# Kernel optimization log

Measured on AMD Instinct MI355X. Metric: run time of the kernel, lower is better.

## Reference

```python
import jax, jax.numpy as jnp
import numpy as np

HEAD = 8

def _mvn(x, eps=1e-5):
    # per-(batch,channel) mean/std over spatial dims; torch .var default is unbiased (ddof=1)
    mean = jnp.mean(x, axis=(2, 3), keepdims=True)
    var = jnp.var(x, axis=(2, 3), ddof=1, keepdims=True) + eps
    return (x - mean) / jnp.sqrt(var)

def _conv1x1(x, w, b):
    return jnp.einsum('bchw,oc->bohw', x, w) + b[None, :, None, None]

def _block_heads(x, p):
    # non-overlapping unfold (kernel==stride==p): pure reshape; matches torch unfold ordering
    b, c, h, w = x.shape
    y = x.reshape(b, c, h // p, p, w // p, p).transpose(0, 1, 2, 4, 3, 5)
    n, r = (h // p) * (w // p), p * p
    return y.reshape(b, HEAD, c // HEAD, n, r)

def _unblock(x, p, h, w):
    # inverse of non-overlapping unfold (fold with kernel==stride)
    b, c, n, r = x.shape
    y = x.reshape(b, c, h // p, w // p, p, p).transpose(0, 1, 2, 4, 3, 5)
    return y.reshape(b, c, h, w)

def setup_inputs() -> dict:
    key = jax.random.key(0)
    ks = jax.random.split(key, 12)
    B, C, H, W = 4, 512, 64, 64
    wmat = lambda k: jax.random.normal(k, (C, C), jnp.float32) * 0.05
    zb = jnp.zeros((C,), jnp.float32)
    return {
        'content': jax.random.normal(ks[0], (B, C, H, W), jnp.float32),
        'style': jax.random.normal(ks[1], (B, C, H, W), jnp.float32),
        'q_w': wmat(ks[2]), 'q_b': zb,
        'k_w': wmat(ks[3]), 'k_b': zb,
        'v_w': wmat(ks[4]), 'v_b': zb,
        'q2_w': wmat(ks[5]), 'q2_b': zb,
        'k2_w': wmat(ks[6]), 'k2_b': zb,
        'v2_w': wmat(ks[7]), 'v2_b': zb,
        'f1_w': wmat(ks[8]), 'f1_b': zb,
        'f2_w': wmat(ks[9]), 'f2_b': zb,
        'sim_alpha': jnp.ones((1,), jnp.float32),
        'sim_beta': jnp.zeros((1,), jnp.float32),
        'layer': 3,
    }

def reference(content, style, q_w, q_b, k_w, k_b, v_w, v_b, q2_w, q2_b, k2_w, k2_b,
              v2_w, v2_b, f1_w, f1_b, f2_w, f2_b, sim_alpha, sim_beta, layer):
    region = 8 if int(layer) in (3, 4) else 4
    b, c, h, w = content.shape
    nc = _mvn(content)
    ns = _mvn(style)
    DA_q = _block_heads(_conv1x1(nc, q_w, q_b), region)      # [b,H,ch,n,r]
    DA_k = _block_heads(_conv1x1(ns, k_w, k_b), region)
    DA_v = _block_heads(_conv1x1(style, v_w, v_b), region)
    PA_q = _block_heads(_conv1x1(nc, q2_w, q2_b), region)
    PA_k = _block_heads(_conv1x1(ns, k2_w, k2_b), region)
    PA_v = _block_heads(_conv1x1(style, v2_w, v2_b), region)
    r = region * region
    n = DA_q.shape[3]
    # --- distinctiveness attention: mean-center clustering + sigmoid-weighted aggregation ---
    DA_k_c = jnp.mean(DA_k, axis=-1)                          # [b,H,ch,n]
    DA_v_c = jnp.mean(DA_v, axis=-1)
    dis = jnp.einsum('bhcx,bhcxy->bhxy', DA_k_c, DA_k)
    sim = jax.nn.sigmoid(sim_beta + sim_alpha * dis)          # [b,H,n,r]
    DA_k_agg = (jnp.einsum('bhxy,bhcxy->bhcx', sim, DA_k) + DA_k_c) / (r + 1)
    DA_v_agg = (jnp.einsum('bhxy,bhcxy->bhcx', sim, DA_v) + DA_v_c) / (r + 1)
    logits = jnp.einsum('bhcxy,bhcz->bhyxz', DA_q, DA_k_agg)  # [b,H,r,n,n]
    scores = jax.nn.softmax(logits, axis=-1)
    DA = jnp.einsum('bhyxz,bhcz->bhcxy', scores, DA_v_agg)    # [b,H,ch,n,r]
    DA_ub = _unblock(DA.reshape(b, c, n, r), region, h, w)
    # --- point attention: argmax NN block matching, then intra-block attention ---
    PA1 = jnp.einsum('bhcxy,bhczy->bhxz', PA_q, PA_k)         # [b,H,n,n]
    idx = jnp.argmax(PA1, axis=-1)                            # [b,H,n]
    idx_b = jnp.broadcast_to(idx[:, :, None, :, None], PA_k.shape)
    PA_k_rs = jnp.take_along_axis(PA_k, idx_b, axis=3)
    PA_v_rs = jnp.take_along_axis(PA_v, idx_b, axis=3)
    logits2 = jnp.einsum('bhcxy,bhcxz->bhxyz', PA_q, PA_k_rs) # [b,H,n,r,r]
    scores2 = jax.nn.softmax(logits2, axis=-1)
    PA = jnp.einsum('bhxyz,bhcxz->bhcxy', scores2, PA_v_rs)
    PA_ub = _unblock(PA.reshape(b, c, n, r), region, h, w)
    O = _conv1x1(DA_ub, f1_w, f1_b) + _conv1x1(PA_ub, f2_w, f2_b)
    return O + content
```

## Files before the change

### kernel.cpp

```cpp
#include <hip/hip_runtime.h>

typedef unsigned short u16;
typedef unsigned int   u32;
typedef _Float16       f16;

typedef f16   f16x8 __attribute__((ext_vector_type(8)));
typedef f16   f16x4 __attribute__((ext_vector_type(4)));
typedef float f32x4 __attribute__((ext_vector_type(4)));

__device__ __forceinline__ f32x4 mfma16(f16x8 a, f16x8 b, f32x4 c){
  return __builtin_amdgcn_mfma_f32_16x16x32_f16(a, b, c, 0, 0, 0);
}

__device__ __forceinline__ void glds16(const f16* g, f16* l){
  __builtin_amdgcn_global_load_lds(
      (const __attribute__((address_space(1))) void*)g,
      (__attribute__((address_space(3))) void*)l, 16, 0, 0);
}

__global__ __launch_bounds__(256) void k_mvn_stats(
    const float* __restrict__ content, const float* __restrict__ style,
    float* __restrict__ stats)
{
  const int src = blockIdx.x >> 11;
  const int row = blockIdx.x & 2047;
  const float* xp = (src ? style : content) + (size_t)row * 4096;
  const int t = threadIdx.x;
  double s = 0.0, ss = 0.0;
  for(int i = t * 4; i < 4096; i += 1024){
    float4 v = *(const float4*)(xp + i);
    s  += (double)v.x + (double)v.y + (double)v.z + (double)v.w;
    ss += (double)v.x * v.x + (double)v.y * v.y + (double)v.z * v.z + (double)v.w * v.w;
  }
  #pragma unroll
  for(int off = 32; off > 0; off >>= 1){
    s  += __shfl_xor(s, off);
    ss += __shfl_xor(ss, off);
  }
  __shared__ double sh[8];
  const int wid = t >> 6;
  if((t & 63) == 0){ sh[wid] = s; sh[4 + wid] = ss; }
  __syncthreads();
  if(t == 0){
    double S  = sh[0] + sh[1] + sh[2] + sh[3];
    double SS = sh[4] + sh[5] + sh[6] + sh[7];
    float mean = (float)(S * (1.0 / 4096.0));
    float var  = (float)((SS - S * S * (1.0 / 4096.0)) * (1.0 / 4095.0));
    stats[src * 4096 + row] = mean;
    stats[src * 4096 + 2048 + row] = rsqrtf(var + 1e-5f);
  }
}

__global__ __launch_bounds__(256) void k_prep_w_all(
    const float* __restrict__ qW,  const float* __restrict__ qB,
    const float* __restrict__ kW,  const float* __restrict__ kB,
    const float* __restrict__ q2W, const float* __restrict__ q2B,
    const float* __restrict__ k2W, const float* __restrict__ k2B,
    const float* __restrict__ vW,  const float* __restrict__ vB,
    const float* __restrict__ v2W, const float* __restrict__ v2B,
    const float* __restrict__ f1W, const float* __restrict__ f2W,
    const float* __restrict__ stats,
    f16* __restrict__ qw, f16* __restrict__ kw,
    f16* __restrict__ q2wh, f16* __restrict__ q2wl,
    f16* __restrict__ k2wh, f16* __restrict__ k2wl,
    f16* __restrict__ vw, f16* __restrict__ v2w,
    f16* __restrict__ f1w, f16* __restrict__ f2w,
    float* __restrict__ biasp)
{
  const int t = threadIdx.x;
  int rid = blockIdx.x * 32 + (t >> 3);
  const float *W; const float *B = nullptr;
  int side = -1, b = 0, o;
  f16 *oh; f16 *ol = nullptr; float* bs = nullptr;
  if(rid < 2048){
    b = rid >> 9; o = rid & 511;
    W = qW; B = qB; side = 0;
    oh = qw + (size_t)(b * 512 + o) * 512;
    bs = biasp + 0 * 2048 + b * 512 + o;
  } else if(rid < 4096){
    rid -= 2048; b = rid >> 9; o = rid & 511;
    W = kW; B = kB; side = 1;
    oh = kw + (size_t)(b * 512 + o) * 512;
    bs = biasp + 1 * 2048 + b * 512 + o;
  } else if(rid < 6144){
    rid -= 4096; b = rid >> 9; o = rid & 511;
    W = q2W; B = q2B; side = 0;
    oh = q2wh + (size_t)(b * 512 + o) * 512;
    ol = q2wl + (size_t)(b * 512 + o) * 512;
    bs = biasp + 4 * 2048 + b * 512 + o;
  } else if(rid < 8192){
    rid -= 6144; b = rid >> 9; o = rid & 511;
    W = k2W; B = k2B; side = 1;
    oh = k2wh + (size_t)(b * 512 + o) * 512;
    ol = k2wl + (size_t)(b * 512 + o) * 512;
    bs = biasp + 5 * 2048 + b * 512 + o;
  } else if(rid < 8704){
    o = rid - 8192; W = vW; B = vB;
    oh = vw + (size_t)o * 512;
    bs = biasp + 2 * 2048 + o;
  } else if(rid < 9216){
    o = rid - 8704; W = v2W; B = v2B;
    oh = v2w + (size_t)o * 512;
    bs = biasp + 3 * 2048 + o;
  } else if(rid < 9728){
    o = rid - 9216; W = f1W;
    oh = f1w + (size_t)o * 512;
  } else {
    o = rid - 9728; W = f2W;
    oh = f2w + (size_t)o * 512;
  }
  const float* mp = (side >= 0) ? stats + side * 4096 + b * 512 : nullptr;
  const float* rp = (side >= 0) ? mp + 2048 : nullptr;
  const int c0 = (t & 7) * 64;
  float dot = 0.f;
  #pragma unroll
  for(int i = 0; i < 64; i += 8){
    int c = c0 + i;
    float w[8];
    *(float4*)(w)     = *(const float4*)(W + (size_t)o * 512 + c);
    *(float4*)(w + 4) = *(const float4*)(W + (size_t)o * 512 + c + 4);
    f16x8 h8, l8;
    #pragma unroll
    for(int j = 0; j < 8; j++){
      float wp = w[j];
      if(side >= 0){
        float r = rp[c + j];
        dot += wp * mp[c + j] * r;
        wp *= r;
      }
      f16 h = (f16)wp;
      h8[j] = h; l8[j] = (f16)(wp - (float)h);
    }
    *(f16x8*)(oh + c) = h8;
    if(ol) *(f16x8*)(ol + c) = l8;
  }
  if(bs){
    dot += __shfl_xor(dot, 1); dot += __shfl_xor(dot, 2); dot += __shfl_xor(dot, 4);
    if((t & 7) == 0) *bs = B[o] - dot;
  }
}

__global__ __launch_bounds__(256) void k_prep_x(
    const float* __restrict__ content, const float* __restrict__ style,
    f16* __restrict__ cth, f16* __restrict__ ctl,
    f16* __restrict__ sth, f16* __restrict__ stl)
{
  const int side = blockIdx.z;
  const int b = blockIdx.y;
  const int s0 = blockIdx.x * 128;
  const float* Xb = (side ? style : content) + (size_t)b * 512 * 4096;
  f16* Oh = (side ? sth : cth) + (size_t)b * 4096 * 512;
  f16* Ol = (side ? stl : ctl) + (size_t)b * 4096 * 512;
  __shared__ float Xs[32][132];
  const int t = threadIdx.x;
  const int s = t >> 1, half = t & 1;
  for(int cc = 0; cc < 512; cc += 32){
    __syncthreads();
    #pragma unroll
    for(int u = 0; u < 4; u++){
      int q = t + u * 256;
      int row = q >> 5, f4 = q & 31;
      float4 v = *(const float4*)(Xb + (size_t)(cc + row) * 4096 + s0 + f4 * 4);
      *(float4*)(&Xs[row][f4 * 4]) = v;
    }
    __syncthreads();
    f16x8 h0, h1, l0, l1;
    #pragma unroll
    for(int i = 0; i < 8; i++){
      float x = Xs[half * 16 + i][s];
      f16 h = (f16)x; h0[i] = h; l0[i] = (f16)(x - (float)h);
    }
    #pragma unroll
    for(int i = 0; i < 8; i++){
      float x = Xs[half * 16 + 8 + i][s];
      f16 h = (f16)x; h1[i] = h; l1[i] = (f16)(x - (float)h);
    }
    size_t o = (size_t)(s0 + s) * 512 + cc + half * 16;
    *(f16x8*)(Oh + o) = h0; *(f16x8*)(Oh + o + 8) = h1;
    *(f16x8*)(Ol + o) = l0; *(f16x8*)(Ol + o + 8) = l1;
  }
}

__global__ __launch_bounds__(256) void k_convT(
    const f16* __restrict__ Xt, const f16* __restrict__ Wp,
    const float* __restrict__ bias, int bw, f16* __restrict__ Out)
{
  const int b = blockIdx.z;
  const int o0 = blockIdx.y * 128;
  const int s0 = blockIdx.x * 128;
  const f16* Xb = Xt + (size_t)b * 4096 * 512;
  const f16* Wb = Wp + (bw ? (size_t)b * 262144 : 0);
  const float* bp = bias + (bw ? b * 512 : 0);
  f16* Ob = Out + (size_t)b * 512 * 4096;
  __shared__ f16 As[4096];
  __shared__ f16 Bs[4096];
  const int t = threadIdx.x;
  const int lane = t & 63, wid = t >> 6;
  const int wm = (wid >> 1) * 64, wn = (wid & 1) * 64;
  const int lr = lane & 15, lg = lane >> 4;
  const int sr = lane >> 2, sc = lane & 3;
  f32x4 acc[4][4] = {};
  for(int kk = 0; kk < 512; kk += 32){
    __syncthreads();
    #pragma unroll
    for(int i = 0; i < 2; i++){
      int r0 = wid * 32 + i * 16;
      int r = r0 + sr;
      int cs = (sc ^ ((r >> 1) & 3)) << 3;
      glds16(Wb + (size_t)(o0 + r) * 512 + kk + cs, As + r0 * 32);
      glds16(Xb + (size_t)(s0 + r) * 512 + kk + cs, Bs + r0 * 32);
    }
    __syncthreads();
    f16x8 av[4], bv[4];
    #pragma unroll
    for(int mi = 0; mi < 4; mi++){
      int row = wm + mi * 16 + lr;
      av[mi] = *(const f16x8*)(As + row * 32 + ((lg ^ ((row >> 1) & 3)) << 3));
    }
    #pragma unroll
    for(int ni = 0; ni < 4; ni++){
      int row = wn + ni * 16 + lr;
      bv[ni] = *(const f16x8*)(Bs + row * 32 + ((lg ^ ((row >> 1) & 3)) << 3));
    }
    #pragma unroll
    for(int mi = 0; mi < 4; mi++){
      #pragma unroll
      for(int ni = 0; ni < 4; ni++)
        acc[mi][ni] = mfma16(av[mi], bv[ni], acc[mi][ni]);
    }
  }
  #pragma unroll
  for(int mi = 0; mi < 4; mi++){
    #pragma unroll
    for(int ni = 0; ni < 4; ni++){
      #pragma unroll
      for(int j = 0; j < 4; j++){
        int o = o0 + wm + mi * 16 + lg * 4 + j;
        int s = s0 + wn + ni * 16 + lr;
        Ob[(size_t)o * 4096 + s] = (f16)(acc[mi][ni][j] + bp[o]);
      }
    }
  }
}

__global__ __launch_bounds__(256) void k_conv3out(
    const f16* __restrict__ Xt,
    const f16* __restrict__ Wk, const f16* __restrict__ Wv, const f16* __restrict__ Wv2,
    const float* __restrict__ biasp,
    f16* __restrict__ Ok, f16* __restrict__ Ov, f16* __restrict__ Ov2)
{
  const int b = blockIdx.z;
  const int seg = blockIdx.y >> 2;
  const int o0 = (blockIdx.y & 3) * 128;
  const int s0 = blockIdx.x * 128;
  const f16* Xb = Xt + (size_t)b * 4096 * 512;
  const f16* Wb = seg == 0 ? Wk + (size_t)b * 262144 : (seg == 1 ? Wv : Wv2);
  const float* bp = biasp + (seg == 0 ? 1 * 2048 + b * 512 : (seg == 1 ? 2 * 2048 : 3 * 2048));
  f16* Ob = (seg == 0 ? Ok : (seg == 1 ? Ov : Ov2)) + (size_t)b * 512 * 4096;
  __shared__ f16 As[4096];
  __shared__ f16 Bs[4096];
  const int t = threadIdx.x;
  const int lane = t & 63, wid = t >> 6;
  const int wm = (wid >> 1) * 64, wn = (wid & 1) * 64;
  const int lr = lane & 15, lg = lane >> 4;
  const int sr = lane >> 2, sc = lane & 3;
  f32x4 acc[4][4] = {};
  for(int kk = 0; kk < 512; kk += 32){
    __syncthreads();
    #pragma unroll
    for(int i = 0; i < 2; i++){
      int r0 = wid * 32 + i * 16;
      int r = r0 + sr;
      int cs = (sc ^ ((r >> 1) & 3)) << 3;
      glds16(Wb + (size_t)(o0 + r) * 512 + kk + cs, As + r0 * 32);
      glds16(Xb + (size_t)(s0 + r) * 512 + kk + cs, Bs + r0 * 32);
    }
    __syncthreads();
    f16x8 av[4], bv[4];
    #pragma unroll
    for(int mi = 0; mi < 4; mi++){
      int row = wm + mi * 16 + lr;
      av[mi] = *(const f16x8*)(As + row * 32 + ((lg ^ ((row >> 1) & 3)) << 3));
    }
    #pragma unroll
    for(int ni = 0; ni < 4; ni++){
      int row = wn + ni * 16 + lr;
      bv[ni] = *(const f16x8*)(Bs + row * 32 + ((lg ^ ((row >> 1) & 3)) << 3));
    }
    #pragma unroll
    for(int mi = 0; mi < 4; mi++){
      #pragma unroll
      for(int ni = 0; ni < 4; ni++)
        acc[mi][ni] = mfma16(av[mi], bv[ni], acc[mi][ni]);
    }
  }
  #pragma unroll
  for(int mi = 0; mi < 4; mi++){
    #pragma unroll
    for(int ni = 0; ni < 4; ni++){
      #pragma unroll
      for(int j = 0; j < 4; j++){
        int o = o0 + wm + mi * 16 + lg * 4 + j;
        int s = s0 + wn + ni * 16 + lr;
        Ob[(size_t)o * 4096 + s] = (f16)(acc[mi][ni][j] + bp[o]);
      }
    }
  }
}

__global__ __launch_bounds__(256) void k_convT3(
    const f16* __restrict__ Xh, const f16* __restrict__ Xl,
    const f16* __restrict__ Wh, const f16* __restrict__ Wl,
    const float* __restrict__ bias, f16* __restrict__ Oh, f16* __restrict__ Ol)
{
  const int b = blockIdx.z;
  const int o0 = blockIdx.y * 128;
  const int s0 = blockIdx.x * 128;
  const f16* Xhb = Xh + (size_t)b * 4096 * 512;
  const f16* Xlb = Xl + (size_t)b * 4096 * 512;
  const f16* Whb = Wh + (size_t)b * 262144;
  const f16* Wlb = Wl + (size_t)b * 262144;
  const float* bp = bias + b * 512;
  f16* Ohb = Oh + (size_t)b * 512 * 4096;
  f16* Olb = Ol + (size_t)b * 512 * 4096;
  __shared__ f16 Ah[4096], Al[4096], Bh[4096], Bl[4096];
  const int t = threadIdx.x;
  const int lane = t & 63, wid = t >> 6;
  const int wm = (wid >> 1) * 64, wn = (wid & 1) * 64;
  const int lr = lane & 15, lg = lane >> 4;
  const int sr = lane >> 2, sc = lane & 3;
  f32x4 acc[4][4] = {};
  for(int kk = 0; kk < 512; kk += 32){
    __syncthreads();
    #pragma unroll
    for(int i = 0; i < 2; i++){
      int r0 = wid * 32 + i * 16;
      int r = r0 + sr;
      int cs = (sc ^ ((r >> 1) & 3)) << 3;
      size_t wsrc = (size_t)(o0 + r) * 512 + kk + cs;
      size_t xsrc = (size_t)(s0 + r) * 512 + kk + cs;
      glds16(Whb + wsrc, Ah + r0 * 32);
      glds16(Wlb + wsrc, Al + r0 * 32);
      glds16(Xhb + xsrc, Bh + r0 * 32);
      glds16(Xlb + xsrc, Bl + r0 * 32);
    }
    __syncthreads();
    f16x8 ah[4], alo[4], bh[4], blo[4];
    #pragma unroll
    for(int mi = 0; mi < 4; mi++){
      int row = wm + mi * 16 + lr;
      int off = row * 32 + ((lg ^ ((row >> 1) & 3)) << 3);
      ah[mi]  = *(const f16x8*)(Ah + off);
      alo[mi] = *(const f16x8*)(Al + off);
    }
    #pragma unroll
    for(int ni = 0; ni < 4; ni++){
      int row = wn + ni * 16 + lr;
      int off = row * 32 + ((lg ^ ((row >> 1) & 3)) << 3);
      bh[ni]  = *(const f16x8*)(Bh + off);
      blo[ni] = *(const f16x8*)(Bl + off);
    }
    #pragma unroll
    for(int mi = 0; mi < 4; mi++){
      #pragma unroll
      for(int ni = 0; ni < 4; ni++){
        f32x4 a = acc[mi][ni];
        a = mfma16(ah[mi],  bh[ni],  a);
        a = mfma16(ah[mi],  blo[ni], a);
        a = mfma16(alo[mi], bh[ni],  a);
        acc[mi][ni] = a;
      }
    }
  }
  #pragma unroll
  for(int mi = 0; mi < 4; mi++){
    #pragma unroll
    for(int ni = 0; ni < 4; ni++){
      #pragma unroll
      for(int j = 0; j < 4; j++){
        int o = o0 + wm + mi * 16 + lg * 4 + j;
        int s = s0 + wn + ni * 16 + lr;
        float v = acc[mi][ni][j] + bp[o];
        f16 h = (f16)v;
        Ohb[(size_t)o * 4096 + s] = h;
        Olb[(size_t)o * 4096 + s] = (f16)(v - (float)h);
      }
    }
  }
}

__global__ __launch_bounds__(256) void k_da1(
    const f16* __restrict__ K, const f16* __restrict__ V,
    const float* __restrict__ alpha_p, const float* __restrict__ beta_p,
    float* __restrict__ kagg, float* __restrict__ vagg)
{
  const int hw = blockIdx.x;
  const int xcd = hw & 7, i = hw >> 3;
  const int g = xcd * 32 + (i >> 3);
  const int bh = g >> 3;
  const int x  = (g & 7) * 8 + (i & 7);
  const f16* Kb = K + (size_t)bh * 64 * 4096;
  const f16* Vb = V + (size_t)bh * 64 * 4096;
  __shared__ float kl[64][65];
  __shared__ float vl[64][65];
  __shared__ float kc[64], vc[64], simv[64];
  const int t = threadIdx.x;
  const int c = t >> 2, yp = t & 3;
  const int xb = (x >> 3) * 512 + (x & 7) * 8;
  #pragma unroll
  for(int u = 0; u < 2; u++){
    int yh = yp * 2 + u;
    f16x8 k8 = *(const f16x8*)(Kb + (size_t)c * 4096 + xb + yh * 64);
    f16x8 v8 = *(const f16x8*)(Vb + (size_t)c * 4096 + xb + yh * 64);
    #pragma unroll
    for(int j = 0; j < 8; j++){
      kl[c][yh * 8 + j] = (float)k8[j];
      vl[c][yh * 8 + j] = (float)v8[j];
    }
  }
  __syncthreads();
  float sk = 0.f, sv = 0.f;
  for(int yy = yp * 16; yy < yp * 16 + 16; yy++){ sk += kl[c][yy]; sv += vl[c][yy]; }
  sk += __shfl_xor(sk, 1); sk += __shfl_xor(sk, 2);
  sv += __shfl_xor(sv, 1); sv += __shfl_xor(sv, 2);
  if(yp == 0){ kc[c] = sk * (1.f / 64.f); vc[c] = sv * (1.f / 64.f); }
  __syncthreads();
  const int y = t >> 2, cp = t & 3;
  float d = 0.f;
  for(int cc = cp * 16; cc < cp * 16 + 16; cc++) d += kc[cc] * kl[cc][y];
  d += __shfl_xor(d, 1); d += __shfl_xor(d, 2);
  if(cp == 0) simv[y] = 1.f / (1.f + expf(-(beta_p[0] + alpha_p[0] * d)));
  __syncthreads();
  float ak = 0.f, av = 0.f;
  for(int yy = yp * 16; yy < yp * 16 + 16; yy++){
    float sm = simv[yy];
    ak += sm * kl[c][yy]; av += sm * vl[c][yy];
  }
  ak += __shfl_xor(ak, 1); ak += __shfl_xor(ak, 2);
  av += __shfl_xor(av, 1); av += __shfl_xor(av, 2);
  if(yp == 0){
    size_t o = ((size_t)bh * 64 + x) * 64 + c;
    kagg[o] = (ak + kc[c]) * (1.f / 65.f);
    vagg[o] = (av + vc[c]) * (1.f / 65.f);
  }
}

__global__ __launch_bounds__(256) void k_da2(
    const f16* __restrict__ Q, const float* __restrict__ kagg,
    const float* __restrict__ vagg, f16* __restrict__ OutT)
{
  const int bh = blockIdx.x >> 4;
  const int s0 = (blockIdx.x & 15) << 8;
  const int b_ = bh >> 3, hd = bh & 7;
  const f16* Qb = Q + (size_t)bh * 64 * 4096;
  f16* Ot = OutT + (size_t)b_ * 4096 * 512 + hd * 64;

  __shared__ __align__(16) f16 Qt[256][72];
  __shared__ __align__(16) f16 Kt[64][72];
  __shared__ __align__(16) f16 Vt[64][72];
  const int t = threadIdx.x;
  const int lane = t & 63, w = t >> 6;
  const int lr = lane & 15, lg = lane >> 4;

  {
    const int so = t & 31;
    #pragma unroll
    for(int pass = 0; pass < 8; pass++){
      int c = (t >> 5) + pass * 8;
      f16x8 q8 = *(const f16x8*)(Qb + (size_t)c * 4096 + s0 + so * 8);
      #pragma unroll
      for(int j = 0; j < 8; j++){
        int s = so * 8 + j;
        int col = (((c >> 3) ^ (s & 7)) << 3) | (c & 7);
        Qt[s][col] = q8[j];
      }
    }
  }
  {
    const int z = t >> 2, c0 = (t & 3) * 16;
    #pragma unroll
    for(int u = 0; u < 4; u++){
      float4 v = *(const float4*)(kagg + (size_t)bh * 4096 + z * 64 + c0 + u * 4);
      float vv[4] = {v.x, v.y, v.z, v.w};
      #pragma unroll
      for(int j = 0; j < 4; j++){
        int c = c0 + u * 4 + j;
        int col = (((c >> 3) ^ (z & 7)) << 3) | (c & 7);
        Kt[z][col] = (f16)vv[j];
      }
    }
    #pragma unroll
    for(int u = 0; u < 4; u++){
      float4 v = *(const float4*)(vagg + (size_t)bh * 4096 + z * 64 + c0 + u * 4);
      float vv[4] = {v.x, v.y, v.z, v.w};
      #pragma unroll
      for(int j = 0; j < 4; j++){
        int c = c0 + u * 4 + j;
        int col = (((z >> 3) ^ (c & 7)) << 3) | (z & 7);
        Vt[c][col] = (f16)vv[j];
      }
    }
  }
  __syncthreads();

  f32x4 acc[4][4] = {};
  #pragma unroll
  for(int kc = 0; kc < 2; kc++){
    f16x8 af[4], bf[4];
    #pragma unroll
    for(int mi = 0; mi < 4; mi++){
      int row = w * 64 + mi * 16 + lr;
      af[mi] = *(const f16x8*)(&Qt[row][(((kc * 4 + lg) ^ (row & 7)) << 3)]);
    }
    #pragma unroll
    for(int ni = 0; ni < 4; ni++){
      int row = ni * 16 + lr;
      bf[ni] = *(const f16x8*)(&Kt[row][(((kc * 4 + lg) ^ (row & 7)) << 3)]);
    }
    #pragma unroll
    for(int mi = 0; mi < 4; mi++){
      #pragma unroll
      for(int ni = 0; ni < 4; ni++)
        acc[mi][ni] = mfma16(af[mi], bf[ni], acc[mi][ni]);
    }
  }

  #pragma unroll
  for(int mi = 0; mi < 4; mi++){
    #pragma unroll
    for(int j = 0; j < 4; j++){
      float v0 = acc[mi][0][j], v1 = acc[mi][1][j], v2 = acc[mi][2][j], v3 = acc[mi][3][j];
      float m = fmaxf(fmaxf(v0, v1), fmaxf(v2, v3));
      m = fmaxf(m, __shfl_xor(m, 1)); m = fmaxf(m, __shfl_xor(m, 2));
      m = fmaxf(m, __shfl_xor(m, 4)); m = fmaxf(m, __shfl_xor(m, 8));
      float e0 = expf(v0 - m), e1 = expf(v1 - m), e2 = expf(v2 - m), e3 = expf(v3 - m);
      float sm = e0 + e1 + e2 + e3;
      sm += __shfl_xor(sm, 1); sm += __shfl_xor(sm, 2);
      sm += __shfl_xor(sm, 4); sm += __shfl_xor(sm, 8);
      float inv = 1.f / sm;
      float ev[4] = {e0, e1, e2, e3};
      int row = w * 64 + mi * 16 + lg * 4 + j;
      #pragma unroll
      for(int ni = 0; ni < 4; ni++){
        int z = lr + 16 * ni;
        int col = (((z >> 3) ^ (row & 7)) << 3) | (z & 7);
        Qt[row][col] = (f16)(ev[ni] * inv);
      }
    }
  }

  f32x4 acc2[4][4] = {};
  #pragma unroll
  for(int kc = 0; kc < 2; kc++){
    f16x8 af[4], bf[4];
    #pragma unroll
    for(int mi = 0; mi < 4; mi++){
      int row = w * 64 + mi * 16 + lr;
      af[mi] = *(const f16x8*)(&Qt[row][(((kc * 4 + lg) ^ (row & 7)) << 3)]);
    }
    #pragma unroll
    for(int ni = 0; ni < 4; ni++){
      int row = ni * 16 + lr;
      bf[ni] = *(const f16x8*)(&Vt[row][(((kc * 4 + lg) ^ (row & 7)) << 3)]);
    }
    #pragma unroll
    for(int mi = 0; mi < 4; mi++){
      #pragma unroll
      for(int ni = 0; ni < 4; ni++)
        acc2[mi][ni] = mfma16(af[mi], bf[ni], acc2[mi][ni]);
    }
  }

  #pragma unroll
  for(int mi = 0; mi < 4; mi++){
    #pragma unroll
    for(int j = 0; j < 4; j++){
      size_t srow = (size_t)(s0 + w * 64 + mi * 16 + lg * 4 + j) * 512;
      #pragma unroll
      for(int ni = 0; ni < 4; ni++)
        Ot[srow + ni * 16 + lr] = (f16)acc2[mi][ni][j];
    }
  }
}

__global__ __launch_bounds__(256) void k_pa1(
    const f16* __restrict__ Qh, const f16* __restrict__ Ql,
    const f16* __restrict__ Kh, const f16* __restrict__ Kl,
    float* __restrict__ pa1p)
{
  const int slice = blockIdx.x & 7;
  const int bh = blockIdx.x >> 3;
  const size_t base = (size_t)bh * 64 * 4096;
  __shared__ f16 Ah[2][64][72], Al[2][64][72], Bh[2][64][72], Bl[2][64][72];
  const int t = threadIdx.x;
  const int lane = t & 63, wid = t >> 6;
  const int wm = (wid >> 1) * 32, wn = (wid & 1) * 32;
  const int lr = lane & 15, lg = lane >> 4;
  f32x4 acc[2][2] = {};
  for(int chunk = 0; chunk < 4; chunk++){
    const int c0 = slice * 8 + chunk * 2;
    __syncthreads();
    #pragma unroll
    for(int cc = 0; cc < 2; cc++){
      size_t cbase = base + (size_t)(c0 + cc) * 4096;
      #pragma unroll
      for(int u = 0; u < 2; u++){
        int e = u * 256 + t;
        int x = e >> 3, yh = e & 7;
        size_t src = cbase + (size_t)((x >> 3) * 512 + (x & 7) * 8 + yh * 64);
        int dst = yh * 8;
        *(f16x8*)(&Ah[cc][x][dst]) = *(const f16x8*)(Qh + src);
        *(f16x8*)(&Al[cc][x][dst]) = *(const f16x8*)(Ql + src);
        *(f16x8*)(&Bh[cc][x][dst]) = *(const f16x8*)(Kh + src);
        *(f16x8*)(&Bl[cc][x][dst]) = *(const f16x8*)(Kl + src);
      }
    }
    __syncthreads();
    #pragma unroll
    for(int cc = 0; cc < 2; cc++){
      #pragma unroll
      for(int kc = 0; kc < 2; kc++){
        f16x8 ah[2], alo[2], bh[2], blo[2];
        #pragma unroll
        for(int mi = 0; mi < 2; mi++){
          ah[mi]  = *(const f16x8*)(&Ah[cc][wm + mi * 16 + lr][kc * 32 + lg * 8]);
          alo[mi] = *(const f16x8*)(&Al[cc][wm + mi * 16 + lr][kc * 32 + lg * 8]);
        }
        #pragma unroll
        for(int ni = 0; ni < 2; ni++){
          bh[ni]  = *(const f16x8*)(&Bh[cc][wn + ni * 16 + lr][kc * 32 + lg * 8]);
          blo[ni] = *(const f16x8*)(&Bl[cc][wn + ni * 16 + lr][kc * 32 + lg * 8]);
        }
        #pragma unroll
        for(int mi = 0; mi < 2; mi++){
          #pragma unroll
          for(int ni = 0; ni < 2; ni++){
            f32x4 a = acc[mi][ni];
            a = mfma16(ah[mi],  bh[ni],  a);
            a = mfma16(ah[mi],  blo[ni], a);
            a = mfma16(alo[mi], bh[ni],  a);
            acc[mi][ni] = a;
          }
        }
      }
    }
  }
  float* outp = pa1p + ((size_t)bh * 8 + slice) * 4096;
  #pragma unroll
  for(int mi = 0; mi < 2; mi++){
    #pragma unroll
    for(int ni = 0; ni < 2; ni++){
      #pragma unroll
      for(int j = 0; j < 4; j++){
        int x = wm + mi * 16 + lg * 4 + j;
        int z = wn + ni * 16 + lr;
        outp[x * 64 + z] = acc[mi][ni][j];
      }
    }
  }
}

__global__ __launch_bounds__(64) void k_pa1r(
    const float* __restrict__ pa1p, int* __restrict__ idx)
{
  const int bh = blockIdx.x;
  const int x = threadIdx.x;
  const float* p = pa1p + (size_t)bh * 8 * 4096 + x * 64;
  float best = -1e30f; int bi = 0;
  for(int z = 0; z < 64; z += 4){
    float4 v = *(const float4*)(p + z);
    #pragma unroll
    for(int sl = 1; sl < 8; sl++){
      float4 w = *(const float4*)(p + sl * 4096 + z);
      v.x += w.x; v.y += w.y; v.z += w.z; v.w += w.w;
    }
    if(v.x > best){ best = v.x; bi = z; }
    if(v.y > best){ best = v.y; bi = z + 1; }
    if(v.z > best){ best = v.z; bi = z + 2; }
    if(v.w > best){ best = v.w; bi = z + 3; }
  }
  idx[bh * 64 + x] = bi;
}

__global__ __launch_bounds__(256) void k_pa2(
    const f16* __restrict__ Qh, const f16* __restrict__ Kh,
    const f16* __restrict__ V2, const int* __restrict__ idx, f16* __restrict__ OutT)
{
  const int hw = blockIdx.x;
  const int bh = (hw & 7) * 4 + ((hw >> 3) >> 6);
  const int x  = (hw >> 3) & 63;
  const int b_ = bh >> 3, hd = bh & 7;
  const size_t base = (size_t)bh * 64 * 4096;
  f16* Ot = OutT + (size_t)b_ * 4096 * 512 + hd * 64;

  __shared__ __align__(16) char Ubuf[18432];
  __shared__ f16 Vn[64][72];
  __shared__ f16 Ps[64][72];
  f16   (*Qt)[72] = (f16(*)[72])Ubuf;
  f16   (*Kt)[72] = (f16(*)[72])(Ubuf + 9216);
  float (*Lf)[66] = (float(*)[66])Ubuf;
  float (*Os)[67] = (float(*)[67])Ubuf;

  const int t = threadIdx.x;
  const int lane = t & 63, wid = t >> 6;
  const int wm = (wid >> 1) * 32, wn = (wid & 1) * 32;
  const int lr = lane & 15, lg = lane >> 4;

  const int xk = idx[bh * 64 + x];
  const int xb = (x >> 3) * 512 + (x & 7) * 8;
  const int kb = (xk >> 3) * 512 + (xk & 7) * 8;

  {
    const int c = t >> 2, q4 = t & 3;
    #pragma unroll
    for(int u = 0; u < 2; u++){
      int yh = q4 * 2 + u;
      f16x8 q8 = *(const f16x8*)(Qh + base + (size_t)c * 4096 + xb + yh * 64);
      f16x8 k8 = *(const f16x8*)(Kh + base + (size_t)c * 4096 + kb + yh * 64);
      f16x8 v8 = *(const f16x8*)(V2 + base + (size_t)c * 4096 + kb + yh * 64);
      int col = ((((c >> 3) ^ yh) & 7) << 3) + (c & 7);
      #pragma unroll
      for(int j = 0; j < 8; j++){
        Qt[yh * 8 + j][col] = q8[j];
        Kt[yh * 8 + j][col] = k8[j];
      }
      *(f16x8*)(&Vn[c][yh * 8]) = v8;
    }
  }
  __syncthreads();

  f32x4 acc[2][2] = {};
  #pragma unroll
  for(int kc = 0; kc < 2; kc++){
    f16x8 af[2], bf[2];
    #pragma unroll
    for(int mi = 0; mi < 2; mi++){
      int row = wm + mi * 16 + lr;
      af[mi] = *(const f16x8*)(&Qt[row][((((kc * 4 + lg) ^ (row >> 3)) & 7) << 3)]);
    }
    #pragma unroll
    for(int ni = 0; ni < 2; ni++){
      int row = wn + ni * 16 + lr;
      bf[ni] = *(const f16x8*)(&Kt[row][((((kc * 4 + lg) ^ (row >> 3)) & 7) << 3)]);
    }
    #pragma unroll
    for(int mi = 0; mi < 2; mi++){
      #pragma unroll
      for(int ni = 0; ni < 2; ni++)
        acc[mi][ni] = mfma16(af[mi], bf[ni], acc[mi][ni]);
    }
  }
  __syncthreads();
  #pragma unroll
  for(int mi = 0; mi < 2; mi++){
    #pragma unroll
    for(int ni = 0; ni < 2; ni++){
      #pragma unroll
      for(int j = 0; j < 4; j++)
        Lf[wm + mi * 16 + lg * 4 + j][wn + ni * 16 + lr] = acc[mi][ni][j];
    }
  }
  __syncthreads();

  {
    const int y = t >> 2, zp = t & 3;
    float l[16];
    #pragma unroll
    for(int i = 0; i < 16; i++) l[i] = Lf[y][zp * 16 + i];
    float m = l[0];
    #pragma unroll
    for(int i = 1; i < 16; i++) m = fmaxf(m, l[i]);
    m = fmaxf(m, __shfl_xor(m, 1)); m = fmaxf(m, __shfl_xor(m, 2));
    float sum = 0.f;
    #pragma unroll
    for(int i = 0; i < 16; i++){ l[i] = expf(l[i] - m); sum += l[i]; }
    sum += __shfl_xor(sum, 1); sum += __shfl_xor(sum, 2);
    float inv = 1.f / sum;
    f16x8 p0, p1;
    #pragma unroll
    for(int i = 0; i < 8; i++){ p0[i] = (f16)(l[i] * inv); p1[i] = (f16)(l[8 + i] * inv); }
    *(f16x8*)(&Ps[y][zp * 16]) = p0;
    *(f16x8*)(&Ps[y][zp * 16 + 8]) = p1;
  }
  __syncthreads();

  f32x4 acc2[2][2] = {};
  #pragma unroll
  for(int kc = 0; kc < 2; kc++){
    f16x8 af[2], bf[2];
    #pragma unroll
    for(int mi = 0; mi < 2; mi++)
      af[mi] = *(const f16x8*)(&Ps[wm + mi * 16 + lr][kc * 32 + lg * 8]);
    #pragma unroll
    for(int ni = 0; ni < 2; ni++)
      bf[ni] = *(const f16x8*)(&Vn[wn + ni * 16 + lr][kc * 32 + lg * 8]);
    #pragma unroll
    for(int mi = 0; mi < 2; mi++){
      #pragma unroll
      for(int ni = 0; ni < 2; ni++)
        acc2[mi][ni] = mfma16(af[mi], bf[ni], acc2[mi][ni]);
    }
  }
  #pragma unroll
  for(int mi = 0; mi < 2; mi++){
    #pragma unroll
    for(int ni = 0; ni < 2; ni++){
      #pragma unroll
      for(int j = 0; j < 4; j++)
        Os[wn + ni * 16 + lr][wm + mi * 16 + lg * 4 + j] = acc2[mi][ni][j];
    }
  }
  __syncthreads();

  {
    const int y = t >> 2, cq = (t & 3) * 16;
    size_t srow = (size_t)(xb + (y >> 3) * 64 + (y & 7)) * 512;
    f16x8 w0, w1;
    #pragma unroll
    for(int i = 0; i < 8; i++){ w0[i] = (f16)Os[cq + i][y]; w1[i] = (f16)Os[cq + 8 + i][y]; }
    *(f16x8*)(Ot + srow + cq) = w0;
    *(f16x8*)(Ot + srow + cq + 8) = w1;
  }
}

__global__ __launch_bounds__(256) void k_finalT(
    const f16* __restrict__ X1t, const f16* __restrict__ X2t,
    const f16* __restrict__ W1p, const f16* __restrict__ W2p,
    const float* __restrict__ B1, const float* __restrict__ B2,
    const float* __restrict__ content, float* __restrict__ out)
{
  const int b = blockIdx.z;
  const int o0 = blockIdx.y * 128;
  const int s0 = blockIdx.x * 128;
  __shared__ f16 As[4096];
  __shared__ f16 Bs[4096];
  const int t = threadIdx.x;
  const int lane = t & 63, wid = t >> 6;
  const int wm = (wid >> 1) * 64, wn = (wid & 1) * 64;
  const int lr = lane & 15, lg = lane >> 4;
  const int sr = lane >> 2, sc = lane & 3;
  f32x4 acc[4][4] = {};
  for(int pass = 0; pass < 2; pass++){
    const f16* Xb = (pass ? X2t : X1t) + (size_t)b * 4096 * 512;
    const f16* Wb = pass ? W2p : W1p;
    for(int kk = 0; kk < 512; kk += 32){
      __syncthreads();
      #pragma unroll
      for(int i = 0; i < 2; i++){
        int r0 = wid * 32 + i * 16;
        int r = r0 + sr;
        int cs = (sc ^ ((r >> 1) & 3)) << 3;
        glds16(Wb + (size_t)(o0 + r) * 512 + kk + cs, As + r0 * 32);
        glds16(Xb + (size_t)(s0 + r) * 512 + kk + cs, Bs + r0 * 32);
      }
      __syncthreads();
      f16x8 av[4], bv[4];
      #pragma unroll
      for(int mi = 0; mi < 4; mi++){
        int row = wm + mi * 16 + lr;
        av[mi] = *(const f16x8*)(As + row * 32 + ((lg ^ ((row >> 1) & 3)) << 3));
      }
      #pragma unroll
      for(int ni = 0; ni < 4; ni++){
        int row = wn + ni * 16 + lr;
        bv[ni] = *(const f16x8*)(Bs + row * 32 + ((lg ^ ((row >> 1) & 3)) << 3));
      }
      #pragma unroll
      for(int mi = 0; mi < 4; mi++){
        #pragma unroll
        for(int ni = 0; ni < 4; ni++)
          acc[mi][ni] = mfma16(av[mi], bv[ni], acc[mi][ni]);
      }
    }
  }
  #pragma unroll
  for(int mi = 0; mi < 4; mi++){
    #pragma unroll
    for(int ni = 0; ni < 4; ni++){
      #pragma unroll
      for(int j = 0; j < 4; j++){
        int o = o0 + wm + mi * 16 + lg * 4 + j;
        int s = s0 + wn + ni * 16 + lr;
        size_t gi = ((size_t)b * 512 + o) * 4096 + s;
        out[gi] = acc[mi][ni][j] + B1[o] + B2[o] + content[gi];
      }
    }
  }
}

extern "C" void kernel_launch(void* const* d_in, const int* in_sizes, int n_in,
                              void* d_out, int out_size, void* d_ws, size_t ws_size,
                              hipStream_t stream) {
  (void)in_sizes; (void)n_in; (void)out_size; (void)ws_size;
  const float* content = (const float*)d_in[0];
  const float* style   = (const float*)d_in[1];
  const float* q_w  = (const float*)d_in[2];  const float* q_b  = (const float*)d_in[3];
  const float* k_w  = (const float*)d_in[4];  const float* k_b  = (const float*)d_in[5];
  const float* v_w  = (const float*)d_in[6];  const float* v_b  = (const float*)d_in[7];
  const float* q2_w = (const float*)d_in[8];  const float* q2_b = (const float*)d_in[9];
  const float* k2_w = (const float*)d_in[10]; const float* k2_b = (const float*)d_in[11];
  const float* v2_w = (const float*)d_in[12]; const float* v2_b = (const float*)d_in[13];
  const float* f1_w = (const float*)d_in[14]; const float* f1_b = (const float*)d_in[15];
  const float* f2_w = (const float*)d_in[16]; const float* f2_b = (const float*)d_in[17];
  const float* sim_alpha = (const float*)d_in[18];
  const float* sim_beta  = (const float*)d_in[19];

  char* ws = (char*)d_ws;
  #define SLOT(i) (ws + (size_t)(i) * 16777216)
  f16* cth = (f16*)SLOT(0);
  f16* ctl = (f16*)SLOT(1);
  f16* sth = (f16*)SLOT(2);
  f16* stl = (f16*)SLOT(3);
  f16* wbase = (f16*)SLOT(4);
  f16* qw   = wbase;
  f16* kw   = wbase + 1 * 1048576;
  f16* q2wh = wbase + 2 * 1048576;
  f16* q2wl = wbase + 3 * 1048576;
  f16* k2wh = wbase + 4 * 1048576;
  f16* k2wl = wbase + 5 * 1048576;
  f16* vw   = wbase + 6 * 1048576;
  f16* v2w  = vw + 262144;
  f16* f1w  = vw + 524288;
  f16* f2w  = vw + 786432;
  f16*   q2h   = (f16*)SLOT(5);
  f16*   q2l   = (f16*)SLOT(6);
  f16*   k2h   = (f16*)SLOT(7);
  f16*   k2l   = (f16*)SLOT(0);
  f16*   qbuf  = (f16*)SLOT(1);
  float* pa1p  = (float*)SLOT(3);
  f16*   kbuf  = (f16*)SLOT(6);
  f16*   vbuf  = (f16*)SLOT(3);
  f16*   v2buf = (f16*)SLOT(0);
  f16*   da_t  = (f16*)SLOT(3);
  f16*   pa_t  = (f16*)SLOT(6);
  float* stats = (float*)(ws + 134217728);
  float* biasp = (float*)(ws + 134217728 + 32768);
  float* kagg  = (float*)(ws + 134217728 + 32768);
  float* vagg  = (float*)(ws + 134217728 + 557056);
  int*   idxb  = (int*)(ws + 134217728 + 1081344);

  dim3 gconv(32, 4, 4);

  k_mvn_stats<<<4096, 256, 0, stream>>>(content, style, stats);

  k_prep_w_all<<<320, 256, 0, stream>>>(
      q_w, q_b, k_w, k_b, q2_w, q2_b, k2_w, k2_b,
      v_w, v_b, v2_w, v2_b, f1_w, f2_w, stats,
      qw, kw, q2wh, q2wl, k2wh, k2wl, vw, v2w, f1w, f2w, biasp);

  k_prep_x<<<dim3(32,4,2), 256, 0, stream>>>(content, style, cth, ctl, sth, stl);

  k_convT3<<<gconv, 256, 0, stream>>>(cth, ctl, q2wh, q2wl, biasp + 4 * 2048, q2h, q2l);
  k_convT <<<gconv, 256, 0, stream>>>(cth, qw, biasp + 0 * 2048, 1, qbuf);
  k_convT3<<<gconv, 256, 0, stream>>>(sth, stl, k2wh, k2wl, biasp + 5 * 2048, k2h, k2l);
  k_pa1<<<256, 256, 0, stream>>>(q2h, q2l, k2h, k2l, pa1p);
  k_pa1r<<<32, 64, 0, stream>>>(pa1p, idxb);
  k_conv3out<<<dim3(32,12,4), 256, 0, stream>>>(sth, kw, vw, v2w, biasp,
                                                kbuf, vbuf, v2buf);

  k_da1<<<2048, 256, 0, stream>>>(kbuf, vbuf, sim_alpha, sim_beta, kagg, vagg);
  k_da2<<<512, 256, 0, stream>>>(qbuf, kagg, vagg, da_t);
  k_pa2<<<2048, 256, 0, stream>>>(q2h, k2h, v2buf, idxb, pa_t);

  k_finalT<<<gconv, 256, 0, stream>>>(da_t, pa_t, f1w, f2w, f1_b, f2_b,
                                      content, (float*)d_out);
}
```

Before: 306.9 us.

## Double-buffer LDS tiles in conv GEMM kernels to overlap loads with MFMA

Converts the four 1x1-conv GEMM kernels (k_convT, k_conv3out, k_convT3, k_finalT) from single-buffered LDS staging to a two-stage ping-pong pipeline. The next K-slice is issued via global_load_lds before computing on the current one, with a partial vmcnt wait so the prefetch stays in flight. The aim is to hide global-load latency behind MFMA work. It doubles LDS use per block, which may reduce occupancy, especially in k_convT3 (64 KB), and relies on hand-written waitcnt counts being correct.

```diff
diff --git a/kernel.cpp b/kernel.cpp
--- a/kernel.cpp
+++ b/kernel.cpp
@@ -16,6 +16,11 @@
   __builtin_amdgcn_global_load_lds(
       (const __attribute__((address_space(1))) void*)g,
       (__attribute__((address_space(3))) void*)l, 16, 0, 0);
+}
+
+__device__ __forceinline__ void barrier_f(){
+  __builtin_amdgcn_s_barrier();
+  asm volatile("" ::: "memory");
 }
 
 __global__ __launch_bounds__(256) void k_mvn_stats(
@@ -192,35 +197,44 @@
   const f16* Wb = Wp + (bw ? (size_t)b * 262144 : 0);
   const float* bp = bias + (bw ? b * 512 : 0);
   f16* Ob = Out + (size_t)b * 512 * 4096;
-  __shared__ f16 As[4096];
-  __shared__ f16 Bs[4096];
+  __shared__ f16 As[2][4096];
+  __shared__ f16 Bs[2][4096];
   const int t = threadIdx.x;
   const int lane = t & 63, wid = t >> 6;
   const int wm = (wid >> 1) * 64, wn = (wid & 1) * 64;
   const int lr = lane & 15, lg = lane >> 4;
   const int sr = lane >> 2, sc = lane & 3;
-  f32x4 acc[4][4] = {};
-  for(int kk = 0; kk < 512; kk += 32){
-    __syncthreads();
+  auto STAGE = [&](int d, int kk){
     #pragma unroll
     for(int i = 0; i < 2; i++){
       int r0 = wid * 32 + i * 16;
-      int r = r0 + sr;
-      int cs = (sc ^ ((r >> 1) & 3)) << 3;
-      glds16(Wb + (size_t)(o0 + r) * 512 + kk + cs, As + r0 * 32);
-      glds16(Xb + (size_t)(s0 + r) * 512 + kk + cs, Bs + r0 * 32);
-    }
-    __syncthreads();
+      int rr = r0 + sr;
+      int cs = (sc ^ ((rr >> 1) & 3)) << 3;
+      glds16(Wb + (size_t)(o0 + rr) * 512 + kk + cs, As[d] + r0 * 32);
+      glds16(Xb + (size_t)(s0 + rr) * 512 + kk + cs, Bs[d] + r0 * 32);
+    }
+  };
+  f32x4 acc[4][4] = {};
+  STAGE(0, 0);
+  int db = 0;
+  for(int tt = 0; tt < 16; tt++){
+    if(tt < 15){
+      STAGE(db ^ 1, (tt + 1) * 32);
+      asm volatile("s_waitcnt vmcnt(4)" ::: "memory");
+    } else {
+      asm volatile("s_waitcnt vmcnt(0)" ::: "memory");
+    }
+    barrier_f();
     f16x8 av[4], bv[4];
     #pragma unroll
     for(int mi = 0; mi < 4; mi++){
       int row = wm + mi * 16 + lr;
-      av[mi] = *(const f16x8*)(As + row * 32 + ((lg ^ ((row >> 1) & 3)) << 3));
+      av[mi] = *(const f16x8*)(As[db] + row * 32 + ((lg ^ ((row >> 1) & 3)) << 3));
     }
     #pragma unroll
     for(int ni = 0; ni < 4; ni++){
       int row = wn + ni * 16 + lr;
-      bv[ni] = *(const f16x8*)(Bs + row * 32 + ((lg ^ ((row >> 1) & 3)) << 3));
+      bv[ni] = *(const f16x8*)(Bs[db] + row * 32 + ((lg ^ ((row >> 1) & 3)) << 3));
     }
     #pragma unroll
     for(int mi = 0; mi < 4; mi++){
@@ -228,6 +242,8 @@
       for(int ni = 0; ni < 4; ni++)
         acc[mi][ni] = mfma16(av[mi], bv[ni], acc[mi][ni]);
     }
+    barrier_f();
+    db ^= 1;
   }
   #pragma unroll
   for(int mi = 0; mi < 4; mi++){
@@ -257,35 +273,44 @@
   const f16* Wb = seg == 0 ? Wk + (size_t)b * 262144 : (seg == 1 ? Wv : Wv2);
   const float* bp = biasp + (seg == 0 ? 1 * 2048 + b * 512 : (seg == 1 ? 2 * 2048 : 3 * 2048));
   f16* Ob = (seg == 0 ? Ok : (seg == 1 ? Ov : Ov2)) + (size_t)b * 512 * 4096;
-  __shared__ f16 As[4096];
-  __shared__ f16 Bs[4096];
+  __shared__ f16 As[2][4096];
+  __shared__ f16 Bs[2][4096];
   const int t = threadIdx.x;
   const int lane = t & 63, wid = t >> 6;
   const int wm = (wid >> 1) * 64, wn = (wid & 1) * 64;
   const int lr = lane & 15, lg = lane >> 4;
   const int sr = lane >> 2, sc = lane & 3;
-  f32x4 acc[4][4] = {};
-  for(int kk = 0; kk < 512; kk += 32){
-    __syncthreads();
+  auto STAGE = [&](int d, int kk){
     #pragma unroll
     for(int i = 0; i < 2; i++){
       int r0 = wid * 32 + i * 16;
-      int r = r0 + sr;
-      int cs = (sc ^ ((r >> 1) & 3)) << 3;
-      glds16(Wb + (size_t)(o0 + r) * 512 + kk + cs, As + r0 * 32);
-      glds16(Xb + (size_t)(s0 + r) * 512 + kk + cs, Bs + r0 * 32);
-    }
-    __syncthreads();
+      int rr = r0 + sr;
+      int cs = (sc ^ ((rr >> 1) & 3)) << 3;
+      glds16(Wb + (size_t)(o0 + rr) * 512 + kk + cs, As[d] + r0 * 32);
+      glds16(Xb + (size_t)(s0 + rr) * 512 + kk + cs, Bs[d] + r0 * 32);
+    }
+  };
+  f32x4 acc[4][4] = {};
+  STAGE(0, 0);
+  int db = 0;
+  for(int tt = 0; tt < 16; tt++){
+    if(tt < 15){
+      STAGE(db ^ 1, (tt + 1) * 32);
+      asm volatile("s_waitcnt vmcnt(4)" ::: "memory");
+    } else {
+      asm volatile("s_waitcnt vmcnt(0)" ::: "memory");
+    }
+    barrier_f();
     f16x8 av[4], bv[4];
     #pragma unroll
     for(int mi = 0; mi < 4; mi++){
       int row = wm + mi * 16 + lr;
-      av[mi] = *(const f16x8*)(As + row * 32 + ((lg ^ ((row >> 1) & 3)) << 3));
+      av[mi] = *(const f16x8*)(As[db] + row * 32 + ((lg ^ ((row >> 1) & 3)) << 3));
     }
     #pragma unroll
     for(int ni = 0; ni < 4; ni++){
       int row = wn + ni * 16 + lr;
-      bv[ni] = *(const f16x8*)(Bs + row * 32 + ((lg ^ ((row >> 1) & 3)) << 3));
+      bv[ni] = *(const f16x8*)(Bs[db] + row * 32 + ((lg ^ ((row >> 1) & 3)) << 3));
     }
     #pragma unroll
     for(int mi = 0; mi < 4; mi++){
@@ -293,6 +318,8 @@
       for(int ni = 0; ni < 4; ni++)
         acc[mi][ni] = mfma16(av[mi], bv[ni], acc[mi][ni]);
     }
+    barrier_f();
+    db ^= 1;
   }
   #pragma unroll
   for(int mi = 0; mi < 4; mi++){
@@ -323,42 +350,51 @@
   const float* bp = bias + b * 512;
   f16* Ohb = Oh + (size_t)b * 512 * 4096;
   f16* Olb = Ol + (size_t)b * 512 * 4096;
-  __shared__ f16 Ah[4096], Al[4096], Bh[4096], Bl[4096];
+  __shared__ f16 Ah[2][4096], Al[2][4096], Bh[2][4096], Bl[2][4096];
   const int t = threadIdx.x;
   const int lane = t & 63, wid = t >> 6;
   const int wm = (wid >> 1) * 64, wn = (wid & 1) * 64;
   const int lr = lane & 15, lg = lane >> 4;
   const int sr = lane >> 2, sc = lane & 3;
-  f32x4 acc[4][4] = {};
-  for(int kk = 0; kk < 512; kk += 32){
-    __syncthreads();
+  auto STAGE = [&](int d, int kk){
     #pragma unroll
     for(int i = 0; i < 2; i++){
       int r0 = wid * 32 + i * 16;
-      int r = r0 + sr;
-      int cs = (sc ^ ((r >> 1) & 3)) << 3;
-      size_t wsrc = (size_t)(o0 + r) * 512 + kk + cs;
-      size_t xsrc = (size_t)(s0 + r) * 512 + kk + cs;
-      glds16(Whb + wsrc, Ah + r0 * 32);
-      glds16(Wlb + wsrc, Al + r0 * 32);
-      glds16(Xhb + xsrc, Bh + r0 * 32);
-      glds16(Xlb + xsrc, Bl + r0 * 32);
-    }
-    __syncthreads();
+      int rr = r0 + sr;
+      int cs = (sc ^ ((rr >> 1) & 3)) << 3;
+      size_t wsrc = (size_t)(o0 + rr) * 512 + kk + cs;
+      size_t xsrc = (size_t)(s0 + rr) * 512 + kk + cs;
+      glds16(Whb + wsrc, Ah[d] + r0 * 32);
+      glds16(Wlb + wsrc, Al[d] + r0 * 32);
+      glds16(Xhb + xsrc, Bh[d] + r0 * 32);
+      glds16(Xlb + xsrc, Bl[d] + r0 * 32);
+    }
+  };
+  f32x4 acc[4][4] = {};
+  STAGE(0, 0);
+  int db = 0;
+  for(int tt = 0; tt < 16; tt++){
+    if(tt < 15){
+      STAGE(db ^ 1, (tt + 1) * 32);
+      asm volatile("s_waitcnt vmcnt(8)" ::: "memory");
+    } else {
+      asm volatile("s_waitcnt vmcnt(0)" ::: "memory");
+    }
+    barrier_f();
     f16x8 ah[4], alo[4], bh[4], blo[4];
     #pragma unroll
     for(int mi = 0; mi < 4; mi++){
       int row = wm + mi * 16 + lr;
       int off = row * 32 + ((lg ^ ((row >> 1) & 3)) << 3);
-      ah[mi]  = *(const f16x8*)(Ah + off);
-      alo[mi] = *(const f16x8*)(Al + off);
+      ah[mi]  = *(const f16x8*)(Ah[db] + off);
+      alo[mi] = *(const f16x8*)(Al[db] + off);
     }
     #pragma unroll
     for(int ni = 0; ni < 4; ni++){
       int row = wn + ni * 16 + lr;
       int off = row * 32 + ((lg ^ ((row >> 1) & 3)) << 3);
-      bh[ni]  = *(const f16x8*)(Bh + off);
-      blo[ni] = *(const f16x8*)(Bl + off);
+      bh[ni]  = *(const f16x8*)(Bh[db] + off);
+      blo[ni] = *(const f16x8*)(Bl[db] + off);
     }
     #pragma unroll
     for(int mi = 0; mi < 4; mi++){
@@ -371,6 +407,8 @@
         acc[mi][ni] = a;
       }
     }
+    barrier_f();
+    db ^= 1;
   }
   #pragma unroll
   for(int mi = 0; mi < 4; mi++){
@@ -832,46 +870,58 @@
   const int b = blockIdx.z;
   const int o0 = blockIdx.y * 128;
   const int s0 = blockIdx.x * 128;
-  __shared__ f16 As[4096];
-  __shared__ f16 Bs[4096];
+  __shared__ f16 As[2][4096];
+  __shared__ f16 Bs[2][4096];
   const int t = threadIdx.x;
   const int lane = t & 63, wid = t >> 6;
   const int wm = (wid >> 1) * 64, wn = (wid & 1) * 64;
   const int lr = lane & 15, lg = lane >> 4;
   const int sr = lane >> 2, sc = lane & 3;
+  const f16* Xp[2] = {X1t + (size_t)b * 4096 * 512, X2t + (size_t)b * 4096 * 512};
+  const f16* Wq[2] = {W1p, W2p};
+  auto STAGE = [&](int d, int tt){
+    const f16* Xb = Xp[tt >> 4];
+    const f16* Wb = Wq[tt >> 4];
+    int kk = (tt & 15) * 32;
+    #pragma unroll
+    for(int i = 0; i < 2; i++){
+      int r0 = wid * 32 + i * 16;
+      int rr = r0 + sr;
+      int cs = (sc ^ ((rr >> 1) & 3)) << 3;
+      glds16(Wb + (size_t)(o0 + rr) * 512 + kk + cs, As[d] + r0 * 32);
+      glds16(Xb + (size_t)(s0 + rr) * 512 + kk + cs, Bs[d] + r0 * 32);
+    }
+  };
   f32x4 acc[4][4] = {};
-  for(int pass = 0; pass < 2; pass++){
-    const f16* Xb = (pass ? X2t : X1t) + (size_t)b * 4096 * 512;
-    const f16* Wb = pass ? W2p : W1p;
-    for(int kk = 0; kk < 512; kk += 32){
-      __syncthreads();
-      #pragma unroll
-      for(int i = 0; i < 2; i++){
-        int r0 = wid * 32 + i * 16;
-        int r = r0 + sr;
-        int cs = (sc ^ ((r >> 1) & 3)) << 3;
-        glds16(Wb + (size_t)(o0 + r) * 512 + kk + cs, As + r0 * 32);
-        glds16(Xb + (size_t)(s0 + r) * 512 + kk + cs, Bs + r0 * 32);
-      }
-      __syncthreads();
-      f16x8 av[4], bv[4];
-      #pragma unroll
-      for(int mi = 0; mi < 4; mi++){
-        int row = wm + mi * 16 + lr;
-        av[mi] = *(const f16x8*)(As + row * 32 + ((lg ^ ((row >> 1) & 3)) << 3));
-      }
-      #pragma unroll
-      for(int ni = 0; ni < 4; ni++){
-        int row = wn + ni * 16 + lr;
-        bv[ni] = *(const f16x8*)(Bs + row * 32 + ((lg ^ ((row >> 1) & 3)) << 3));
-      }
-      #pragma unroll
-      for(int mi = 0; mi < 4; mi++){
-        #pragma unroll
-        for(int ni = 0; ni < 4; ni++)
-          acc[mi][ni] = mfma16(av[mi], bv[ni], acc[mi][ni]);
-      }
-    }
+  STAGE(0, 0);
+  int db = 0;
+  for(int tt = 0; tt < 32; tt++){
+    if(tt < 31){
+      STAGE(db ^ 1, tt + 1);
+      asm volatile("s_waitcnt vmcnt(4)" ::: "memory");
+    } else {
+      asm volatile("s_waitcnt vmcnt(0)" ::: "memory");
+    }
+    barrier_f();
+    f16x8 av[4], bv[4];
+    #pragma unroll
+    for(int mi = 0; mi < 4; mi++){
+      int row = wm + mi * 16 + lr;
+      av[mi] = *(const f16x8*)(As[db] + row * 32 + ((lg ^ ((row >> 1) & 3)) << 3));
+    }
+    #pragma unroll
+    for(int ni = 0; ni < 4; ni++){
+      int row = wn + ni * 16 + lr;
+      bv[ni] = *(const f16x8*)(Bs[db] + row * 32 + ((lg ^ ((row >> 1) & 3)) << 3));
+    }
+    #pragma unroll
+    for(int mi = 0; mi < 4; mi++){
+      #pragma unroll
+      for(int ni = 0; ni < 4; ni++)
+        acc[mi][ni] = mfma16(av[mi], bv[ni], acc[mi][ni]);
+    }
+    barrier_f();
+    db ^= 1;
   }
   #pragma unroll
   for(int mi = 0; mi < 4; mi++){
```

New measurement: 310.4 us. Within noise of the previous version (+1.1%).
